# Kernel optimization log

Measured on AMD Instinct MI355X. Metric: run time of the kernel, lower is better.

The kernel has to match this reference:

```python
import jax, jax.numpy as jnp
import numpy as np

H1, H2 = 32, 16  # LSTM units per direction (layer 1, layer 2)
F = 64           # input feature dim


def lstm(x, W, U, b, reverse=False, return_sequences=True):
    """Keras-style LSTM. x: [B,T,F]. W:[F,4H], U:[H,4H], b:[4H].
    Gate order i,f,g,o; sigmoid recurrent activation, tanh activation.
    Dropout is inference-mode (identity). If reverse, process time backwards
    (go_backwards=True)."""
    if reverse:
        x = x[:, ::-1]
    B = x.shape[0]
    H = U.shape[0]
    xW = jnp.einsum('btf,fg->btg', x, W) + b  # [B,T,4H] precomputed input gates

    def step(carry, xw_t):
        h, c = carry
        z = xw_t + h @ U                       # [B,4H]
        i, f, g, o = jnp.split(z, 4, axis=-1)
        i = jax.nn.sigmoid(i)
        f = jax.nn.sigmoid(f)
        g = jnp.tanh(g)
        o = jax.nn.sigmoid(o)
        c = f * c + i * g
        h = o * jnp.tanh(c)
        return (h, c), h

    h0 = jnp.zeros((B, H), x.dtype)
    (h_last, _), hs = jax.lax.scan(step, (h0, h0), jnp.swapaxes(xW, 0, 1))
    if return_sequences:
        hs = jnp.swapaxes(hs, 0, 1)  # [B,T,H]
        if reverse:
            hs = hs[:, ::-1]  # Bidirectional re-reverses backward outputs
        return hs
    return h_last


def setup_inputs() -> dict:
    key = jax.random.key(0)
    ks = jax.random.split(key, 17)
    s = 0.05
    d = {
        'inputs': jax.random.normal(ks[0], (4096, 128, F), jnp.float32),
        # layer 1 (bidirectional, 32 units each dir)
        'W1f': jax.random.normal(ks[1], (F, 4 * H1)) * s,
        'U1f': jax.random.normal(ks[2], (H1, 4 * H1)) * s,
        'b1f': jnp.zeros((4 * H1,)),
        'W1b': jax.random.normal(ks[3], (F, 4 * H1)) * s,
        'U1b': jax.random.normal(ks[4], (H1, 4 * H1)) * s,
        'b1b': jnp.zeros((4 * H1,)),
        # layer 2 (bidirectional, 16 units each dir, input 2*H1=64)
        'W2f': jax.random.normal(ks[5], (2 * H1, 4 * H2)) * s,
        'U2f': jax.random.normal(ks[6], (H2, 4 * H2)) * s,
        'b2f': jnp.zeros((4 * H2,)),
        'W2b': jax.random.normal(ks[7], (2 * H1, 4 * H2)) * s,
        'U2b': jax.random.normal(ks[8], (H2, 4 * H2)) * s,
        'b2b': jnp.zeros((4 * H2,)),
        # dense head
        'W3': jax.random.normal(ks[9], (2 * H2, 8)) * s,
        'b3': jnp.zeros((8,)),
        'W4': jax.random.normal(ks[10], (8, 2)) * s,
        'b4': jnp.zeros((2,)),
    }
    return d


def reference(inputs, W1f, U1f, b1f, W1b, U1b, b1b,
              W2f, U2f, b2f, W2b, U2b, b2b, W3, b3, W4, b4):
    # bi_one: concat(forward seq, time-aligned backward seq) -> [B,T,64]
    h1f = lstm(inputs, W1f, U1f, b1f, reverse=False, return_sequences=True)
    h1b = lstm(inputs, W1b, U1b, b1b, reverse=True, return_sequences=True)
    x = jnp.concatenate([h1f, h1b], axis=-1)
    # bi_two: last hidden state of each direction -> [B,32]
    h2f = lstm(x, W2f, U2f, b2f, reverse=False, return_sequences=False)
    h2b = lstm(x, W2b, U2b, b2b, reverse=True, return_sequences=False)
    x = jnp.concatenate([h2f, h2b], axis=-1)
    x = x @ W3 + b3
    x = x * jax.nn.sigmoid(x)  # swish
    x = x @ W4 + b4
    return jax.nn.sigmoid(x)
```

## Files before the change

### kernel.cpp

```cpp
#include <hip/hip_runtime.h>
#include <hip/hip_bf16.h>

#define T 128
#define F 64
#define H1 32
#define G1 128
#define H2 16
#define G2 64

typedef __attribute__((ext_vector_type(8))) short bf16x8;
typedef __attribute__((ext_vector_type(4))) float f32x4;

__device__ __forceinline__ float sigmoidf_(float x) {
    return 1.0f / (1.0f + __expf(-x));
}
__device__ __forceinline__ float tanhf_(float x) {
    return 1.0f - 2.0f / (__expf(2.0f * x) + 1.0f);
}
__device__ __forceinline__ unsigned short f2bf(float f) {
    union { float f; unsigned u; } c; c.f = f;
    unsigned r = c.u + 0x7FFF + ((c.u >> 16) & 1);
    return (unsigned short)(r >> 16);
}
__device__ __forceinline__ void lds_barrier() {
    asm volatile("s_waitcnt lgkmcnt(0)" ::: "memory");
    __builtin_amdgcn_s_barrier();
}

__global__ __launch_bounds__(256) void xcvt(
    const float* __restrict__ x,
    unsigned short* __restrict__ xbf)
{
    __shared__ unsigned short tile[1024];
    const int g  = blockIdx.x;
    const int t0 = blockIdx.y * 8;
    const int m  = threadIdx.x >> 4;
    const int c4 = threadIdx.x & 15;
    const int ks   = c4 >> 3;
    const int quad = (c4 & 7) >> 1;
    const int j0   = (c4 & 1) * 4;
    const int slot = ks * 512 + (m + 16 * quad) * 8 + j0;

    for (int tt = 0; tt < 8; ++tt) {
        const int t = t0 + tt;
        const float4 v = *(const float4*)(x + ((size_t)(g * 16 + m) * T + t) * 64 + c4 * 4);
        ushort4 u;
        u.x = f2bf(v.x); u.y = f2bf(v.y); u.z = f2bf(v.z); u.w = f2bf(v.w);
        *(ushort4*)(tile + slot) = u;
        __syncthreads();
        *(uint2*)(xbf + (size_t)(g * T + t) * 1024 + threadIdx.x * 4) =
            *(const uint2*)(tile + threadIdx.x * 4);
        __syncthreads();
    }
}

__global__ __launch_bounds__(256, 2) void lstm1_fused(
    const unsigned short* __restrict__ xbf,
    const float* __restrict__ W1f, const float* __restrict__ b1f, const float* __restrict__ U1f,
    const float* __restrict__ W1b, const float* __restrict__ b1b, const float* __restrict__ U1b,
    unsigned short* __restrict__ h1)
{
    __shared__ unsigned short hb[2][16 * 40];
    const int tid  = threadIdx.x;
    const int lane = tid & 63;
    const int wv   = __builtin_amdgcn_readfirstlane(tid >> 6);
    const int gh   = wv & 1;
    const int sh   = wv >> 1;
    const int n15  = lane & 15, quad = lane >> 4;
    const int d    = blockIdx.x & 1, g = blockIdx.x >> 1;

    const float* W  = d ? W1b : W1f;
    const float* U  = d ? U1b : U1f;
    const float* bs = d ? b1b : b1f;

    bf16x8 Wf[4][2], Uf[4];
    f32x4 biasC[4];
    #pragma unroll
    for (int i = 0; i < 4; ++i) {
        const int col = (2 * i + gh) * 16 + n15;
        biasC[i] = (f32x4)(bs[col]);
        #pragma unroll
        for (int ks = 0; ks < 2; ++ks) {
            bf16x8 f;
            #pragma unroll
            for (int j = 0; j < 8; ++j)
                f[j] = (short)f2bf(W[(ks * 32 + quad * 8 + j) * G1 + col]);
            Wf[i][ks] = f;
        }
        bf16x8 u;
        #pragma unroll
        for (int j = 0; j < 8; ++j)
            u[j] = (short)f2bf(U[(quad * 8 + j) * G1 + col]);
        Uf[i] = u;
    }

    #pragma unroll
    for (int i = 0; i < 5; ++i) ((unsigned short*)hb)[tid + i * 256] = 0;

    float c0 = 0.0f, c1 = 0.0f;
    const unsigned short* xb = xbf + (size_t)g * T * 1024 + lane * 8;
    unsigned short* h1b0 = h1 + (size_t)g * T * 1024
        + d * 512 + ((quad * 4 + 2 * sh) + 16 * (gh * 2 + (n15 >> 3))) * 8 + (n15 & 7);
    unsigned short* h1b1 = h1b0 + 8;

    bf16x8 xA0, xA1, xB0, xB1;
    {
        const unsigned short* p0 = xb + (size_t)(d ? (T - 1) : 0) * 1024;
        xA0 = *(const bf16x8*)(p0); xA1 = *(const bf16x8*)(p0 + 512);
        const unsigned short* p1 = xb + (size_t)(d ? (T - 2) : 1) * 1024;
        xB0 = *(const bf16x8*)(p1); xB1 = *(const bf16x8*)(p1 + 512);
    }
    lds_barrier();

    auto step = [&](int s, bf16x8& x0, bf16x8& x1) {
        const int t = d ? (T - 1 - s) : s;
        f32x4 a0 = __builtin_amdgcn_mfma_f32_16x16x32_bf16(x0, Wf[0][0], biasC[0], 0, 0, 0);
        f32x4 a1 = __builtin_amdgcn_mfma_f32_16x16x32_bf16(x0, Wf[1][0], biasC[1], 0, 0, 0);
        f32x4 a2 = __builtin_amdgcn_mfma_f32_16x16x32_bf16(x0, Wf[2][0], biasC[2], 0, 0, 0);
        f32x4 a3 = __builtin_amdgcn_mfma_f32_16x16x32_bf16(x0, Wf[3][0], biasC[3], 0, 0, 0);
        a0 = __builtin_amdgcn_mfma_f32_16x16x32_bf16(x1, Wf[0][1], a0, 0, 0, 0);
        a1 = __builtin_amdgcn_mfma_f32_16x16x32_bf16(x1, Wf[1][1], a1, 0, 0, 0);
        a2 = __builtin_amdgcn_mfma_f32_16x16x32_bf16(x1, Wf[2][1], a2, 0, 0, 0);
        a3 = __builtin_amdgcn_mfma_f32_16x16x32_bf16(x1, Wf[3][1], a3, 0, 0, 0);

        if (s + 2 < T) {
            const unsigned short* pn = xb + (size_t)(d ? (T - 3 - s) : (s + 2)) * 1024;
            x0 = *(const bf16x8*)(pn); x1 = *(const bf16x8*)(pn + 512);
        }

        const bf16x8 af = *(const bf16x8*)(hb[s & 1] + n15 * 40 + quad * 8);
        a0 = __builtin_amdgcn_mfma_f32_16x16x32_bf16(af, Uf[0], a0, 0, 0, 0);
        a1 = __builtin_amdgcn_mfma_f32_16x16x32_bf16(af, Uf[1], a1, 0, 0, 0);
        a2 = __builtin_amdgcn_mfma_f32_16x16x32_bf16(af, Uf[2], a2, 0, 0, 0);
        a3 = __builtin_amdgcn_mfma_f32_16x16x32_bf16(af, Uf[3], a3, 0, 0, 0);

        {
            const float ig = sigmoidf_(sh ? a0[2] : a0[0]);
            const float fg = sigmoidf_(sh ? a1[2] : a1[0]);
            const float gg = tanhf_(sh ? a2[2] : a2[0]);
            const float og = sigmoidf_(sh ? a3[2] : a3[0]);
            c0 = fg * c0 + ig * gg;
            const float h = og * tanhf_(c0);
            const unsigned short us = f2bf(h);
            hb[(s + 1) & 1][(quad * 4 + 2 * sh) * 40 + gh * 16 + n15] = us;
            h1b0[(size_t)t * 1024] = us;
        }
        {
            const float ig = sigmoidf_(sh ? a0[3] : a0[1]);
            const float fg = sigmoidf_(sh ? a1[3] : a1[1]);
            const float gg = tanhf_(sh ? a2[3] : a2[1]);
            const float og = sigmoidf_(sh ? a3[3] : a3[1]);
            c1 = fg * c1 + ig * gg;
            const float h = og * tanhf_(c1);
            const unsigned short us = f2bf(h);
            hb[(s + 1) & 1][(quad * 4 + 2 * sh + 1) * 40 + gh * 16 + n15] = us;
            h1b1[(size_t)t * 1024] = us;
        }
        lds_barrier();
    };

    #pragma unroll 1
    for (int s = 0; s < T; s += 2) {
        step(s, xA0, xA1);
        step(s + 1, xB0, xB1);
    }
}

__global__ __launch_bounds__(512, 2) void lstm2_head(
    const unsigned short* __restrict__ h1,
    const float* __restrict__ W2f, const float* __restrict__ b2f, const float* __restrict__ U2f,
    const float* __restrict__ W2b, const float* __restrict__ b2b, const float* __restrict__ U2b,
    const float* __restrict__ W3, const float* __restrict__ b3,
    const float* __restrict__ W4, const float* __restrict__ b4,
    float* __restrict__ out)
{
    __shared__ unsigned short hb2[2][2][400];
    __shared__ float hfin[2][16][16];
    __shared__ float ybuf[16][9];
    const int tid  = threadIdx.x;
    const int lane = tid & 63;
    const int wv   = __builtin_amdgcn_readfirstlane(tid >> 6);
    const int d    = wv & 1;
    const int sh   = wv >> 1;
    const int n15  = lane & 15, quad = lane >> 4;
    const int g    = blockIdx.x;

    const float* W  = d ? W2b : W2f;
    const float* U  = d ? U2b : U2f;
    const float* bs = d ? b2b : b2f;

    bf16x8 Wf[4][2], Uf[4];
    f32x4 biasC[4];
    #pragma unroll
    for (int i = 0; i < 4; ++i) {
        const int col = i * 16 + n15;
        biasC[i] = (f32x4)(bs[col]);
        #pragma unroll
        for (int ks = 0; ks < 2; ++ks) {
            bf16x8 f;
            #pragma unroll
            for (int j = 0; j < 8; ++j)
                f[j] = (short)f2bf(W[(ks * 32 + quad * 8 + j) * G2 + col]);
            Wf[i][ks] = f;
        }
        bf16x8 u;
        #pragma unroll
        for (int j = 0; j < 8; ++j) {
            const int k = quad * 8 + j;
            u[j] = (k < H2) ? (short)f2bf(U[k * G2 + col]) : (short)0;
        }
        Uf[i] = u;
    }

    #pragma unroll
    for (int i = 0; i < 4; ++i) {
        const int idx = tid + i * 512;
        if (idx < 1600) ((unsigned short*)hb2)[idx] = 0;
    }

    float c = 0.0f, hlast = 0.0f;
    const unsigned short* hl = h1 + (size_t)g * T * 1024 + lane * 8;

    bf16x8 hA0, hA1, hB0, hB1;
    {
        const unsigned short* p0 = hl + (size_t)(d ? (T - 1) : 0) * 1024;
        hA0 = *(const bf16x8*)(p0); hA1 = *(const bf16x8*)(p0 + 512);
        const unsigned short* p1 = hl + (size_t)(d ? (T - 2) : 1) * 1024;
        hB0 = *(const bf16x8*)(p1); hB1 = *(const bf16x8*)(p1 + 512);
    }
    lds_barrier();

    auto step = [&](int s, bf16x8& x0, bf16x8& x1) {
        f32x4 a0 = __builtin_amdgcn_mfma_f32_16x16x32_bf16(x0, Wf[0][0], biasC[0], 0, 0, 0);
        f32x4 a1 = __builtin_amdgcn_mfma_f32_16x16x32_bf16(x0, Wf[1][0], biasC[1], 0, 0, 0);
        f32x4 a2 = __builtin_amdgcn_mfma_f32_16x16x32_bf16(x0, Wf[2][0], biasC[2], 0, 0, 0);
        f32x4 a3 = __builtin_amdgcn_mfma_f32_16x16x32_bf16(x0, Wf[3][0], biasC[3], 0, 0, 0);
        a0 = __builtin_amdgcn_mfma_f32_16x16x32_bf16(x1, Wf[0][1], a0, 0, 0, 0);
        a1 = __builtin_amdgcn_mfma_f32_16x16x32_bf16(x1, Wf[1][1], a1, 0, 0, 0);
        a2 = __builtin_amdgcn_mfma_f32_16x16x32_bf16(x1, Wf[2][1], a2, 0, 0, 0);
        a3 = __builtin_amdgcn_mfma_f32_16x16x32_bf16(x1, Wf[3][1], a3, 0, 0, 0);

        if (s + 2 < T) {
            const unsigned short* pn = hl + (size_t)(d ? (T - 3 - s) : (s + 2)) * 1024;
            x0 = *(const bf16x8*)(pn); x1 = *(const bf16x8*)(pn + 512);
        }

        const bf16x8 af = *(const bf16x8*)(hb2[d][s & 1] + n15 * 24 + quad * 8);
        a0 = __builtin_amdgcn_mfma_f32_16x16x32_bf16(af, Uf[0], a0, 0, 0, 0);
        a1 = __builtin_amdgcn_mfma_f32_16x16x32_bf16(af, Uf[1], a1, 0, 0, 0);
        a2 = __builtin_amdgcn_mfma_f32_16x16x32_bf16(af, Uf[2], a2, 0, 0, 0);
        a3 = __builtin_amdgcn_mfma_f32_16x16x32_bf16(af, Uf[3], a3, 0, 0, 0);

        const float z0 = (sh & 1) ? ((sh & 2) ? a0[3] : a0[1]) : ((sh & 2) ? a0[2] : a0[0]);
        const float z1 = (sh & 1) ? ((sh & 2) ? a1[3] : a1[1]) : ((sh & 2) ? a1[2] : a1[0]);
        const float z2 = (sh & 1) ? ((sh & 2) ? a2[3] : a2[1]) : ((sh & 2) ? a2[2] : a2[0]);
        const float z3 = (sh & 1) ? ((sh & 2) ? a3[3] : a3[1]) : ((sh & 2) ? a3[2] : a3[0]);
        const float ig = sigmoidf_(z0);
        const float fg = sigmoidf_(z1);
        const float gg = tanhf_(z2);
        const float og = sigmoidf_(z3);
        c = fg * c + ig * gg;
        hlast = og * tanhf_(c);
        hb2[d][(s + 1) & 1][(quad * 4 + sh) * 24 + n15] = f2bf(hlast);
        lds_barrier();
    };

    #pragma unroll 1
    for (int s = 0; s < T; s += 2) {
        step(s, hA0, hA1);
        step(s + 1, hB0, hB1);
    }

    hfin[d][quad * 4 + sh][n15] = hlast;
    __syncthreads();

    if (tid < 128) {
        const int s = tid >> 3, u = tid & 7;
        float a = b3[u];
        #pragma unroll
        for (int k = 0; k < H2; ++k) a += hfin[0][s][k] * W3[k * 8 + u];
        #pragma unroll
        for (int k = 0; k < H2; ++k) a += hfin[1][s][k] * W3[(H2 + k) * 8 + u];
        ybuf[s][u] = a * sigmoidf_(a);
    }
    __syncthreads();
    if (tid < 32) {
        const int s = tid >> 1, o = tid & 1;
        float a = b4[o];
        #pragma unroll
        for (int k = 0; k < 8; ++k) a += ybuf[s][k] * W4[k * 2 + o];
        out[(size_t)(g * 16 + s) * 2 + o] = sigmoidf_(a);
    }
}

extern "C" void kernel_launch(void* const* d_in, const int* in_sizes, int n_in,
                              void* d_out, int out_size, void* d_ws, size_t ws_size,
                              hipStream_t stream) {
    const float* x   = (const float*)d_in[0];
    const float* W1f = (const float*)d_in[1];
    const float* U1f = (const float*)d_in[2];
    const float* b1f = (const float*)d_in[3];
    const float* W1b = (const float*)d_in[4];
    const float* U1b = (const float*)d_in[5];
    const float* b1b = (const float*)d_in[6];
    const float* W2f = (const float*)d_in[7];
    const float* U2f = (const float*)d_in[8];
    const float* b2f = (const float*)d_in[9];
    const float* W2b = (const float*)d_in[10];
    const float* U2b = (const float*)d_in[11];
    const float* b2b = (const float*)d_in[12];
    const float* W3  = (const float*)d_in[13];
    const float* b3  = (const float*)d_in[14];
    const float* W4  = (const float*)d_in[15];
    const float* b4  = (const float*)d_in[16];
    float* out = (float*)d_out;

    const int B  = in_sizes[0] / (T * F);
    const int NG = B / 16;

    const size_t perG = (size_t)T * 1024 * sizeof(unsigned short);
    int chG = (int)(ws_size / (2 * perG));
    if (chG > NG) chG = NG;
    if (chG < 1) chG = 1;
    unsigned short* xbf = (unsigned short*)d_ws;
    unsigned short* h1  = xbf + (size_t)chG * T * 1024;

    for (int g0 = 0; g0 < NG; g0 += chG) {
        const int cg = (NG - g0 < chG) ? (NG - g0) : chG;
        dim3 gcv(cg, T / 8);
        xcvt<<<gcv, 256, 0, stream>>>(x + (size_t)g0 * 16 * T * F, xbf);
        lstm1_fused<<<cg * 2, 256, 0, stream>>>(
            xbf, W1f, b1f, U1f, W1b, b1b, U1b, h1);
        lstm2_head<<<cg, 512, 0, stream>>>(
            h1, W2f, b2f, U2f, W2b, b2b, U2b, W3, b3, W4, b4,
            out + (size_t)g0 * 16 * 2);
    }
}
```

Measured before the change: 428.1 us.

## Software-pipeline input projection MFMAs one step ahead of recurrent chain

Both LSTM kernels now compute the input projection x·W for step s+2 while step s's recurrent h·U MFMAs and gate math run. This takes those MFMAs off the serial per-step critical path, and the input prefetch distance grows to four steps. Sigmoid and tanh now use the hardware reciprocal instead of a division, and gate element selection uses branches on sh instead of nested selects. The cost is more accumulator registers per lane and slightly lower precision in the activations.

Result: faster. 383.4 us (-10.4%).

```diff
diff --git a/kernel.cpp b/kernel.cpp
--- a/kernel.cpp
+++ b/kernel.cpp
@@ -12,10 +12,10 @@
 typedef __attribute__((ext_vector_type(4))) float f32x4;
 
 __device__ __forceinline__ float sigmoidf_(float x) {
-    return 1.0f / (1.0f + __expf(-x));
+    return __builtin_amdgcn_rcpf(1.0f + __expf(-x));
 }
 __device__ __forceinline__ float tanhf_(float x) {
-    return 1.0f - 2.0f / (__expf(2.0f * x) + 1.0f);
+    return 1.0f - 2.0f * __builtin_amdgcn_rcpf(__expf(2.0f * x) + 1.0f);
 }
 __device__ __forceinline__ unsigned short f2bf(float f) {
     union { float f; unsigned u; } c; c.f = f;
@@ -103,42 +103,65 @@
         + d * 512 + ((quad * 4 + 2 * sh) + 16 * (gh * 2 + (n15 >> 3))) * 8 + (n15 & 7);
     unsigned short* h1b1 = h1b0 + 8;
 
+    f32x4 xaA[4], xaB[4];
     bf16x8 xA0, xA1, xB0, xB1;
     {
         const unsigned short* p0 = xb + (size_t)(d ? (T - 1) : 0) * 1024;
-        xA0 = *(const bf16x8*)(p0); xA1 = *(const bf16x8*)(p0 + 512);
+        bf16x8 t0 = *(const bf16x8*)(p0), t1 = *(const bf16x8*)(p0 + 512);
+        #pragma unroll
+        for (int i = 0; i < 4; ++i) {
+            xaA[i] = __builtin_amdgcn_mfma_f32_16x16x32_bf16(t0, Wf[i][0], biasC[i], 0, 0, 0);
+            xaA[i] = __builtin_amdgcn_mfma_f32_16x16x32_bf16(t1, Wf[i][1], xaA[i], 0, 0, 0);
+        }
         const unsigned short* p1 = xb + (size_t)(d ? (T - 2) : 1) * 1024;
-        xB0 = *(const bf16x8*)(p1); xB1 = *(const bf16x8*)(p1 + 512);
+        t0 = *(const bf16x8*)(p1); t1 = *(const bf16x8*)(p1 + 512);
+        #pragma unroll
+        for (int i = 0; i < 4; ++i) {
+            xaB[i] = __builtin_amdgcn_mfma_f32_16x16x32_bf16(t0, Wf[i][0], biasC[i], 0, 0, 0);
+            xaB[i] = __builtin_amdgcn_mfma_f32_16x16x32_bf16(t1, Wf[i][1], xaB[i], 0, 0, 0);
+        }
+        const unsigned short* p2 = xb + (size_t)(d ? (T - 3) : 2) * 1024;
+        xA0 = *(const bf16x8*)(p2); xA1 = *(const bf16x8*)(p2 + 512);
+        const unsigned short* p3 = xb + (size_t)(d ? (T - 4) : 3) * 1024;
+        xB0 = *(const bf16x8*)(p3); xB1 = *(const bf16x8*)(p3 + 512);
     }
     lds_barrier();
 
-    auto step = [&](int s, bf16x8& x0, bf16x8& x1) {
+    auto step = [&](int s, f32x4* xa, bf16x8& x0, bf16x8& x1) {
+        const bf16x8 af = *(const bf16x8*)(hb[s & 1] + n15 * 40 + quad * 8);
+        f32x4 a0 = __builtin_amdgcn_mfma_f32_16x16x32_bf16(af, Uf[0], xa[0], 0, 0, 0);
+        f32x4 a1 = __builtin_amdgcn_mfma_f32_16x16x32_bf16(af, Uf[1], xa[1], 0, 0, 0);
+        f32x4 a2 = __builtin_amdgcn_mfma_f32_16x16x32_bf16(af, Uf[2], xa[2], 0, 0, 0);
+        f32x4 a3 = __builtin_amdgcn_mfma_f32_16x16x32_bf16(af, Uf[3], xa[3], 0, 0, 0);
+
+        xa[0] = __builtin_amdgcn_mfma_f32_16x16x32_bf16(x0, Wf[0][0], biasC[0], 0, 0, 0);
+        xa[1] = __builtin_amdgcn_mfma_f32_16x16x32_bf16(x0, Wf[1][0], biasC[1], 0, 0, 0);
+        xa[2] = __builtin_amdgcn_mfma_f32_16x16x32_bf16(x0, Wf[2][0], biasC[2], 0, 0, 0);
+        xa[3] = __builtin_amdgcn_mfma_f32_16x16x32_bf16(x0, Wf[3][0], biasC[3], 0, 0, 0);
+        xa[0] = __builtin_amdgcn_mfma_f32_16x16x32_bf16(x1, Wf[0][1], xa[0], 0, 0, 0);
+        xa[1] = __builtin_amdgcn_mfma_f32_16x16x32_bf16(x1, Wf[1][1], xa[1], 0, 0, 0);
+        xa[2] = __builtin_amdgcn_mfma_f32_16x16x32_bf16(x1, Wf[2][1], xa[2], 0, 0, 0);
+        xa[3] = __builtin_amdgcn_mfma_f32_16x16x32_bf16(x1, Wf[3][1], xa[3], 0, 0, 0);
+
+        if (s + 4 < T) {
+            const unsigned short* pn = xb + (size_t)(d ? (T - 5 - s) : (s + 4)) * 1024;
+            x0 = *(const bf16x8*)(pn); x1 = *(const bf16x8*)(pn + 512);
+        }
+
         const int t = d ? (T - 1 - s) : s;
-        f32x4 a0 = __builtin_amdgcn_mfma_f32_16x16x32_bf16(x0, Wf[0][0], biasC[0], 0, 0, 0);
-        f32x4 a1 = __builtin_amdgcn_mfma_f32_16x16x32_bf16(x0, Wf[1][0], biasC[1], 0, 0, 0);
-        f32x4 a2 = __builtin_amdgcn_mfma_f32_16x16x32_bf16(x0, Wf[2][0], biasC[2], 0, 0, 0);
-        f32x4 a3 = __builtin_amdgcn_mfma_f32_16x16x32_bf16(x0, Wf[3][0], biasC[3], 0, 0, 0);
-        a0 = __builtin_amdgcn_mfma_f32_16x16x32_bf16(x1, Wf[0][1], a0, 0, 0, 0);
-        a1 = __builtin_amdgcn_mfma_f32_16x16x32_bf16(x1, Wf[1][1], a1, 0, 0, 0);
-        a2 = __builtin_amdgcn_mfma_f32_16x16x32_bf16(x1, Wf[2][1], a2, 0, 0, 0);
-        a3 = __builtin_amdgcn_mfma_f32_16x16x32_bf16(x1, Wf[3][1], a3, 0, 0, 0);
-
-        if (s + 2 < T) {
-            const unsigned short* pn = xb + (size_t)(d ? (T - 3 - s) : (s + 2)) * 1024;
-            x0 = *(const bf16x8*)(pn); x1 = *(const bf16x8*)(pn + 512);
-        }
-
-        const bf16x8 af = *(const bf16x8*)(hb[s & 1] + n15 * 40 + quad * 8);
-        a0 = __builtin_amdgcn_mfma_f32_16x16x32_bf16(af, Uf[0], a0, 0, 0, 0);
-        a1 = __builtin_amdgcn_mfma_f32_16x16x32_bf16(af, Uf[1], a1, 0, 0, 0);
-        a2 = __builtin_amdgcn_mfma_f32_16x16x32_bf16(af, Uf[2], a2, 0, 0, 0);
-        a3 = __builtin_amdgcn_mfma_f32_16x16x32_bf16(af, Uf[3], a3, 0, 0, 0);
-
+        float zi0, zi1, zf0, zf1, zg0, zg1, zo0, zo1;
+        if (sh == 0) {
+            zi0 = a0[0]; zi1 = a0[1]; zf0 = a1[0]; zf1 = a1[1];
+            zg0 = a2[0]; zg1 = a2[1]; zo0 = a3[0]; zo1 = a3[1];
+        } else {
+            zi0 = a0[2]; zi1 = a0[3]; zf0 = a1[2]; zf1 = a1[3];
+            zg0 = a2[2]; zg1 = a2[3]; zo0 = a3[2]; zo1 = a3[3];
+        }
         {
-            const float ig = sigmoidf_(sh ? a0[2] : a0[0]);
-            const float fg = sigmoidf_(sh ? a1[2] : a1[0]);
-            const float gg = tanhf_(sh ? a2[2] : a2[0]);
-            const float og = sigmoidf_(sh ? a3[2] : a3[0]);
+            const float ig = sigmoidf_(zi0);
+            const float fg = sigmoidf_(zf0);
+            const float gg = tanhf_(zg0);
+            const float og = sigmoidf_(zo0);
             c0 = fg * c0 + ig * gg;
             const float h = og * tanhf_(c0);
             const unsigned short us = f2bf(h);
@@ -146,10 +169,10 @@
             h1b0[(size_t)t * 1024] = us;
         }
         {
-            const float ig = sigmoidf_(sh ? a0[3] : a0[1]);
-            const float fg = sigmoidf_(sh ? a1[3] : a1[1]);
-            const float gg = tanhf_(sh ? a2[3] : a2[1]);
-            const float og = sigmoidf_(sh ? a3[3] : a3[1]);
+            const float ig = sigmoidf_(zi1);
+            const float fg = sigmoidf_(zf1);
+            const float gg = tanhf_(zg1);
+            const float og = sigmoidf_(zo1);
             c1 = fg * c1 + ig * gg;
             const float h = og * tanhf_(c1);
             const unsigned short us = f2bf(h);
@@ -161,8 +184,8 @@
 
     #pragma unroll 1
     for (int s = 0; s < T; s += 2) {
-        step(s, xA0, xA1);
-        step(s + 1, xB0, xB1);
+        step(s, xaA, xA0, xA1);
+        step(s + 1, xaB, xB0, xB1);
     }
 }
 
@@ -221,40 +244,56 @@
     float c = 0.0f, hlast = 0.0f;
     const unsigned short* hl = h1 + (size_t)g * T * 1024 + lane * 8;
 
+    f32x4 xaA[4], xaB[4];
     bf16x8 hA0, hA1, hB0, hB1;
     {
         const unsigned short* p0 = hl + (size_t)(d ? (T - 1) : 0) * 1024;
-        hA0 = *(const bf16x8*)(p0); hA1 = *(const bf16x8*)(p0 + 512);
+        bf16x8 t0 = *(const bf16x8*)(p0), t1 = *(const bf16x8*)(p0 + 512);
+        #pragma unroll
+        for (int i = 0; i < 4; ++i) {
+            xaA[i] = __builtin_amdgcn_mfma_f32_16x16x32_bf16(t0, Wf[i][0], biasC[i], 0, 0, 0);
+            xaA[i] = __builtin_amdgcn_mfma_f32_16x16x32_bf16(t1, Wf[i][1], xaA[i], 0, 0, 0);
+        }
         const unsigned short* p1 = hl + (size_t)(d ? (T - 2) : 1) * 1024;
-        hB0 = *(const bf16x8*)(p1); hB1 = *(const bf16x8*)(p1 + 512);
+        t0 = *(const bf16x8*)(p1); t1 = *(const bf16x8*)(p1 + 512);
+        #pragma unroll
+        for (int i = 0; i < 4; ++i) {
+            xaB[i] = __builtin_amdgcn_mfma_f32_16x16x32_bf16(t0, Wf[i][0], biasC[i], 0, 0, 0);
+            xaB[i] = __builtin_amdgcn_mfma_f32_16x16x32_bf16(t1, Wf[i][1], xaB[i], 0, 0, 0);
+        }
+        const unsigned short* p2 = hl + (size_t)(d ? (T - 3) : 2) * 1024;
+        hA0 = *(const bf16x8*)(p2); hA1 = *(const bf16x8*)(p2 + 512);
+        const unsigned short* p3 = hl + (size_t)(d ? (T - 4) : 3) * 1024;
+        hB0 = *(const bf16x8*)(p3); hB1 = *(const bf16x8*)(p3 + 512);
     }
     lds_barrier();
 
-    auto step = [&](int s, bf16x8& x0, bf16x8& x1) {
-        f32x4 a0 = __builtin_amdgcn_mfma_f32_16x16x32_bf16(x0, Wf[0][0], biasC[0], 0, 0, 0);
-        f32x4 a1 = __builtin_amdgcn_mfma_f32_16x16x32_bf16(x0, Wf[1][0], biasC[1], 0, 0, 0);
-        f32x4 a2 = __builtin_amdgcn_mfma_f32_16x16x32_bf16(x0, Wf[2][0], biasC[2], 0, 0, 0);
-        f32x4 a3 = __builtin_amdgcn_mfma_f32_16x16x32_bf16(x0, Wf[3][0], biasC[3], 0, 0, 0);
-        a0 = __builtin_amdgcn_mfma_f32_16x16x32_bf16(x1, Wf[0][1], a0, 0, 0, 0);
-        a1 = __builtin_amdgcn_mfma_f32_16x16x32_bf16(x1, Wf[1][1], a1, 0, 0, 0);
-        a2 = __builtin_amdgcn_mfma_f32_16x16x32_bf16(x1, Wf[2][1], a2, 0, 0, 0);
-        a3 = __builtin_amdgcn_mfma_f32_16x16x32_bf16(x1, Wf[3][1], a3, 0, 0, 0);
-
-        if (s + 2 < T) {
-            const unsigned short* pn = hl + (size_t)(d ? (T - 3 - s) : (s + 2)) * 1024;
+    auto step = [&](int s, f32x4* xa, bf16x8& x0, bf16x8& x1) {
+        const bf16x8 af = *(const bf16x8*)(hb2[d][s & 1] + n15 * 24 + quad * 8);
+        f32x4 a0 = __builtin_amdgcn_mfma_f32_16x16x32_bf16(af, Uf[0], xa[0], 0, 0, 0);
+        f32x4 a1 = __builtin_amdgcn_mfma_f32_16x16x32_bf16(af, Uf[1], xa[1], 0, 0, 0);
+        f32x4 a2 = __builtin_amdgcn_mfma_f32_16x16x32_bf16(af, Uf[2], xa[2], 0, 0, 0);
+        f32x4 a3 = __builtin_amdgcn_mfma_f32_16x16x32_bf16(af, Uf[3], xa[3], 0, 0, 0);
+
+        xa[0] = __builtin_amdgcn_mfma_f32_16x16x32_bf16(x0, Wf[0][0], biasC[0], 0, 0, 0);
+        xa[1] = __builtin_amdgcn_mfma_f32_16x16x32_bf16(x0, Wf[1][0], biasC[1], 0, 0, 0);
+        xa[2] = __builtin_amdgcn_mfma_f32_16x16x32_bf16(x0, Wf[2][0], biasC[2], 0, 0, 0);
+        xa[3] = __builtin_amdgcn_mfma_f32_16x16x32_bf16(x0, Wf[3][0], biasC[3], 0, 0, 0);
+        xa[0] = __builtin_amdgcn_mfma_f32_16x16x32_bf16(x1, Wf[0][1], xa[0], 0, 0, 0);
+        xa[1] = __builtin_amdgcn_mfma_f32_16x16x32_bf16(x1, Wf[1][1], xa[1], 0, 0, 0);
+        xa[2] = __builtin_amdgcn_mfma_f32_16x16x32_bf16(x1, Wf[2][1], xa[2], 0, 0, 0);
+        xa[3] = __builtin_amdgcn_mfma_f32_16x16x32_bf16(x1, Wf[3][1], xa[3], 0, 0, 0);
+
+        if (s + 4 < T) {
+            const unsigned short* pn = hl + (size_t)(d ? (T - 5 - s) : (s + 4)) * 1024;
             x0 = *(const bf16x8*)(pn); x1 = *(const bf16x8*)(pn + 512);
         }
 
-        const bf16x8 af = *(const bf16x8*)(hb2[d][s & 1] + n15 * 24 + quad * 8);
-        a0 = __builtin_amdgcn_mfma_f32_16x16x32_bf16(af, Uf[0], a0, 0, 0, 0);
-        a1 = __builtin_amdgcn_mfma_f32_16x16x32_bf16(af, Uf[1], a1, 0, 0, 0);
-        a2 = __builtin_amdgcn_mfma_f32_16x16x32_bf16(af, Uf[2], a2, 0, 0, 0);
-        a3 = __builtin_amdgcn_mfma_f32_16x16x32_bf16(af, Uf[3], a3, 0, 0, 0);
-
-        const float z0 = (sh & 1) ? ((sh & 2) ? a0[3] : a0[1]) : ((sh & 2) ? a0[2] : a0[0]);
-        const float z1 = (sh & 1) ? ((sh & 2) ? a1[3] : a1[1]) : ((sh & 2) ? a1[2] : a1[0]);
-        const float z2 = (sh & 1) ? ((sh & 2) ? a2[3] : a2[1]) : ((sh & 2) ? a2[2] : a2[0]);
-        const float z3 = (sh & 1) ? ((sh & 2) ? a3[3] : a3[1]) : ((sh & 2) ? a3[2] : a3[0]);
+        float z0, z1, z2, z3;
+        if (sh == 0)      { z0 = a0[0]; z1 = a1[0]; z2 = a2[0]; z3 = a3[0]; }
+        else if (sh == 1) { z0 = a0[1]; z1 = a1[1]; z2 = a2[1]; z3 = a3[1]; }
+        else if (sh == 2) { z0 = a0[2]; z1 = a1[2]; z2 = a2[2]; z3 = a3[2]; }
+        else              { z0 = a0[3]; z1 = a1[3]; z2 = a2[3]; z3 = a3[3]; }
         const float ig = sigmoidf_(z0);
         const float fg = sigmoidf_(z1);
         const float gg = tanhf_(z2);
@@ -267,8 +306,8 @@
 
     #pragma unroll 1
     for (int s = 0; s < T; s += 2) {
-        step(s, hA0, hA1);
-        step(s + 1, hB0, hB1);
+        step(s, xaA, hA0, hA1);
+        step(s + 1, xaB, hB0, hB1);
     }
 
     hfin[d][quad * 4 + sh][n15] = hlast;
```

## Interleave two batch groups per LSTM block and split head into its own kernel

Applied to the files above, without the earlier changes.

Each recurrent block now processes two independent 16-sample groups, so the MFMA and activation latency of one group can overlap the other within a single serial timestep. The input projection for the next step is computed after the recurrent MFMA, which takes it off the critical path. Layer 2 is split per direction into 256-thread blocks, and the dense head runs as a separate kernel that reads final states from the workspace. Other changes: the conversion kernel drops its LDS staging, and the activations use reciprocal intrinsics. The trade-offs are fewer blocks overall, occupancy of one block per CU, higher register pressure, and an extra kernel launch.

Measured after the change: 479.5 us. 12.0% more time.

```diff
diff --git a/kernel.cpp b/kernel.cpp
--- a/kernel.cpp
+++ b/kernel.cpp
@@ -11,11 +11,13 @@
 typedef __attribute__((ext_vector_type(8))) short bf16x8;
 typedef __attribute__((ext_vector_type(4))) float f32x4;
 
+#define MFMA __builtin_amdgcn_mfma_f32_16x16x32_bf16
+
 __device__ __forceinline__ float sigmoidf_(float x) {
-    return 1.0f / (1.0f + __expf(-x));
+    return __builtin_amdgcn_rcpf(1.0f + __expf(-x));
 }
 __device__ __forceinline__ float tanhf_(float x) {
-    return 1.0f - 2.0f / (__expf(2.0f * x) + 1.0f);
+    return 1.0f - 2.0f * __builtin_amdgcn_rcpf(__expf(2.0f * x) + 1.0f);
 }
 __device__ __forceinline__ unsigned short f2bf(float f) {
     union { float f; unsigned u; } c; c.f = f;
@@ -31,43 +33,37 @@
     const float* __restrict__ x,
     unsigned short* __restrict__ xbf)
 {
-    __shared__ unsigned short tile[1024];
-    const int g  = blockIdx.x;
-    const int t0 = blockIdx.y * 8;
-    const int m  = threadIdx.x >> 4;
-    const int c4 = threadIdx.x & 15;
-    const int ks   = c4 >> 3;
-    const int quad = (c4 & 7) >> 1;
-    const int j0   = (c4 & 1) * 4;
-    const int slot = ks * 512 + (m + 16 * quad) * 8 + j0;
-
-    for (int tt = 0; tt < 8; ++tt) {
-        const int t = t0 + tt;
-        const float4 v = *(const float4*)(x + ((size_t)(g * 16 + m) * T + t) * 64 + c4 * 4);
-        ushort4 u;
-        u.x = f2bf(v.x); u.y = f2bf(v.y); u.z = f2bf(v.z); u.w = f2bf(v.w);
-        *(ushort4*)(tile + slot) = u;
-        __syncthreads();
-        *(uint2*)(xbf + (size_t)(g * T + t) * 1024 + threadIdx.x * 4) =
-            *(const uint2*)(tile + threadIdx.x * 4);
-        __syncthreads();
-    }
-}
-
-__global__ __launch_bounds__(256, 2) void lstm1_fused(
+    const int g = blockIdx.x;
+    const int t = blockIdx.y * 2 + (threadIdx.x >> 7);
+    const int r = threadIdx.x & 127;
+    const int m = r & 15, ks = (r >> 4) & 1, q = r >> 5;
+    const float* src = x + ((size_t)(g * 16 + m) * T + t) * 64 + ks * 32 + q * 8;
+    const float4 v0 = *(const float4*)src;
+    const float4 v1 = *(const float4*)(src + 4);
+    bf16x8 u;
+    u[0] = (short)f2bf(v0.x); u[1] = (short)f2bf(v0.y);
+    u[2] = (short)f2bf(v0.z); u[3] = (short)f2bf(v0.w);
+    u[4] = (short)f2bf(v1.x); u[5] = (short)f2bf(v1.y);
+    u[6] = (short)f2bf(v1.z); u[7] = (short)f2bf(v1.w);
+    *(bf16x8*)(xbf + (size_t)(g * T + t) * 1024 + ks * 512 + (m + 16 * q) * 8) = u;
+}
+
+__global__ __launch_bounds__(256, 1) void lstm1_fused(
     const unsigned short* __restrict__ xbf,
     const float* __restrict__ W1f, const float* __restrict__ b1f, const float* __restrict__ U1f,
     const float* __restrict__ W1b, const float* __restrict__ b1b, const float* __restrict__ U1b,
-    unsigned short* __restrict__ h1)
+    unsigned short* __restrict__ h1, const int ng)
 {
-    __shared__ unsigned short hb[2][16 * 40];
+    __shared__ unsigned short hb[2][2][640];
     const int tid  = threadIdx.x;
     const int lane = tid & 63;
     const int wv   = __builtin_amdgcn_readfirstlane(tid >> 6);
     const int gh   = wv & 1;
     const int sh   = wv >> 1;
     const int n15  = lane & 15, quad = lane >> 4;
-    const int d    = blockIdx.x & 1, g = blockIdx.x >> 1;
+    const int d    = blockIdx.x & 1, gp = blockIdx.x >> 1;
+    const int g0   = gp * 2;
+    const int g1   = (g0 + 1 < ng) ? (g0 + 1) : g0;
 
     const float* W  = d ? W1b : W1f;
     const float* U  = d ? U1b : U1f;
@@ -95,95 +91,108 @@
     }
 
     #pragma unroll
-    for (int i = 0; i < 5; ++i) ((unsigned short*)hb)[tid + i * 256] = 0;
-
-    float c0 = 0.0f, c1 = 0.0f;
-    const unsigned short* xb = xbf + (size_t)g * T * 1024 + lane * 8;
-    unsigned short* h1b0 = h1 + (size_t)g * T * 1024
-        + d * 512 + ((quad * 4 + 2 * sh) + 16 * (gh * 2 + (n15 >> 3))) * 8 + (n15 & 7);
-    unsigned short* h1b1 = h1b0 + 8;
-
-    bf16x8 xA0, xA1, xB0, xB1;
-    {
-        const unsigned short* p0 = xb + (size_t)(d ? (T - 1) : 0) * 1024;
-        xA0 = *(const bf16x8*)(p0); xA1 = *(const bf16x8*)(p0 + 512);
-        const unsigned short* p1 = xb + (size_t)(d ? (T - 2) : 1) * 1024;
-        xB0 = *(const bf16x8*)(p1); xB1 = *(const bf16x8*)(p1 + 512);
+    for (int i = 0; i < 10; ++i) ((unsigned short*)hb)[tid + i * 256] = 0;
+
+    float c0[2] = {0.f, 0.f}, c1[2] = {0.f, 0.f};
+    const unsigned short* xb[2];
+    unsigned short* hw[2];
+    xb[0] = xbf + (size_t)g0 * T * 1024 + lane * 8;
+    xb[1] = xbf + (size_t)g1 * T * 1024 + lane * 8;
+    const int hoff = d * 512
+        + ((quad * 4 + 2 * sh) + 16 * (gh * 2 + (n15 >> 3))) * 8 + (n15 & 7);
+    hw[0] = h1 + (size_t)g0 * T * 1024 + hoff;
+    hw[1] = h1 + (size_t)g1 * T * 1024 + hoff;
+
+    f32x4 xa[2][4];
+    bf16x8 xP0[2], xP1[2];
+    #pragma unroll
+    for (int S = 0; S < 2; ++S) {
+        const unsigned short* p0 = xb[S] + (size_t)(d ? (T - 1) : 0) * 1024;
+        const bf16x8 t0 = *(const bf16x8*)p0, t1 = *(const bf16x8*)(p0 + 512);
+        #pragma unroll
+        for (int i = 0; i < 4; ++i) {
+            xa[S][i] = MFMA(t0, Wf[i][0], biasC[i], 0, 0, 0);
+            xa[S][i] = MFMA(t1, Wf[i][1], xa[S][i], 0, 0, 0);
+        }
+        const unsigned short* p1 = xb[S] + (size_t)(d ? (T - 2) : 1) * 1024;
+        xP0[S] = *(const bf16x8*)p1;
+        xP1[S] = *(const bf16x8*)(p1 + 512);
     }
     lds_barrier();
 
-    auto step = [&](int s, bf16x8& x0, bf16x8& x1) {
+    #pragma unroll 1
+    for (int s = 0; s < T; ++s) {
         const int t = d ? (T - 1 - s) : s;
-        f32x4 a0 = __builtin_amdgcn_mfma_f32_16x16x32_bf16(x0, Wf[0][0], biasC[0], 0, 0, 0);
-        f32x4 a1 = __builtin_amdgcn_mfma_f32_16x16x32_bf16(x0, Wf[1][0], biasC[1], 0, 0, 0);
-        f32x4 a2 = __builtin_amdgcn_mfma_f32_16x16x32_bf16(x0, Wf[2][0], biasC[2], 0, 0, 0);
-        f32x4 a3 = __builtin_amdgcn_mfma_f32_16x16x32_bf16(x0, Wf[3][0], biasC[3], 0, 0, 0);
-        a0 = __builtin_amdgcn_mfma_f32_16x16x32_bf16(x1, Wf[0][1], a0, 0, 0, 0);
-        a1 = __builtin_amdgcn_mfma_f32_16x16x32_bf16(x1, Wf[1][1], a1, 0, 0, 0);
-        a2 = __builtin_amdgcn_mfma_f32_16x16x32_bf16(x1, Wf[2][1], a2, 0, 0, 0);
-        a3 = __builtin_amdgcn_mfma_f32_16x16x32_bf16(x1, Wf[3][1], a3, 0, 0, 0);
-
-        if (s + 2 < T) {
-            const unsigned short* pn = xb + (size_t)(d ? (T - 3 - s) : (s + 2)) * 1024;
-            x0 = *(const bf16x8*)(pn); x1 = *(const bf16x8*)(pn + 512);
-        }
-
-        const bf16x8 af = *(const bf16x8*)(hb[s & 1] + n15 * 40 + quad * 8);
-        a0 = __builtin_amdgcn_mfma_f32_16x16x32_bf16(af, Uf[0], a0, 0, 0, 0);
-        a1 = __builtin_amdgcn_mfma_f32_16x16x32_bf16(af, Uf[1], a1, 0, 0, 0);
-        a2 = __builtin_amdgcn_mfma_f32_16x16x32_bf16(af, Uf[2], a2, 0, 0, 0);
-        a3 = __builtin_amdgcn_mfma_f32_16x16x32_bf16(af, Uf[3], a3, 0, 0, 0);
-
-        {
-            const float ig = sigmoidf_(sh ? a0[2] : a0[0]);
-            const float fg = sigmoidf_(sh ? a1[2] : a1[0]);
-            const float gg = tanhf_(sh ? a2[2] : a2[0]);
-            const float og = sigmoidf_(sh ? a3[2] : a3[0]);
-            c0 = fg * c0 + ig * gg;
-            const float h = og * tanhf_(c0);
-            const unsigned short us = f2bf(h);
-            hb[(s + 1) & 1][(quad * 4 + 2 * sh) * 40 + gh * 16 + n15] = us;
-            h1b0[(size_t)t * 1024] = us;
-        }
-        {
-            const float ig = sigmoidf_(sh ? a0[3] : a0[1]);
-            const float fg = sigmoidf_(sh ? a1[3] : a1[1]);
-            const float gg = tanhf_(sh ? a2[3] : a2[1]);
-            const float og = sigmoidf_(sh ? a3[3] : a3[1]);
-            c1 = fg * c1 + ig * gg;
-            const float h = og * tanhf_(c1);
-            const unsigned short us = f2bf(h);
-            hb[(s + 1) & 1][(quad * 4 + 2 * sh + 1) * 40 + gh * 16 + n15] = us;
-            h1b1[(size_t)t * 1024] = us;
+        f32x4 a[2][4];
+        #pragma unroll
+        for (int S = 0; S < 2; ++S) {
+            const bf16x8 af = *(const bf16x8*)(hb[S][s & 1] + n15 * 40 + quad * 8);
+            #pragma unroll
+            for (int i = 0; i < 4; ++i)
+                a[S][i] = MFMA(af, Uf[i], xa[S][i], 0, 0, 0);
+        }
+        #pragma unroll
+        for (int S = 0; S < 2; ++S) {
+            #pragma unroll
+            for (int i = 0; i < 4; ++i)
+                xa[S][i] = MFMA(xP0[S], Wf[i][0], biasC[i], 0, 0, 0);
+            #pragma unroll
+            for (int i = 0; i < 4; ++i)
+                xa[S][i] = MFMA(xP1[S], Wf[i][1], xa[S][i], 0, 0, 0);
+            if (s + 2 < T) {
+                const unsigned short* pn =
+                    xb[S] + (size_t)(d ? (T - 3 - s) : (s + 2)) * 1024;
+                xP0[S] = *(const bf16x8*)pn;
+                xP1[S] = *(const bf16x8*)(pn + 512);
+            }
+        }
+        #pragma unroll
+        for (int S = 0; S < 2; ++S) {
+            float zi0, zi1, zf0, zf1, zg0, zg1, zo0, zo1;
+            if (sh == 0) {
+                zi0 = a[S][0][0]; zi1 = a[S][0][1]; zf0 = a[S][1][0]; zf1 = a[S][1][1];
+                zg0 = a[S][2][0]; zg1 = a[S][2][1]; zo0 = a[S][3][0]; zo1 = a[S][3][1];
+            } else {
+                zi0 = a[S][0][2]; zi1 = a[S][0][3]; zf0 = a[S][1][2]; zf1 = a[S][1][3];
+                zg0 = a[S][2][2]; zg1 = a[S][2][3]; zo0 = a[S][3][2]; zo1 = a[S][3][3];
+            }
+            {
+                const float ig = sigmoidf_(zi0), fg = sigmoidf_(zf0);
+                const float gg = tanhf_(zg0),   og = sigmoidf_(zo0);
+                c0[S] = fg * c0[S] + ig * gg;
+                const float h = og * tanhf_(c0[S]);
+                const unsigned short us = f2bf(h);
+                hb[S][(s + 1) & 1][(quad * 4 + 2 * sh) * 40 + gh * 16 + n15] = us;
+                hw[S][(size_t)t * 1024] = us;
+            }
+            {
+                const float ig = sigmoidf_(zi1), fg = sigmoidf_(zf1);
+                const float gg = tanhf_(zg1),   og = sigmoidf_(zo1);
+                c1[S] = fg * c1[S] + ig * gg;
+                const float h = og * tanhf_(c1[S]);
+                const unsigned short us = f2bf(h);
+                hb[S][(s + 1) & 1][(quad * 4 + 2 * sh + 1) * 40 + gh * 16 + n15] = us;
+                hw[S][(size_t)t * 1024 + 8] = us;
+            }
         }
         lds_barrier();
-    };
-
-    #pragma unroll 1
-    for (int s = 0; s < T; s += 2) {
-        step(s, xA0, xA1);
-        step(s + 1, xB0, xB1);
-    }
-}
-
-__global__ __launch_bounds__(512, 2) void lstm2_head(
+    }
+}
+
+__global__ __launch_bounds__(256, 1) void lstm2_rec(
     const unsigned short* __restrict__ h1,
     const float* __restrict__ W2f, const float* __restrict__ b2f, const float* __restrict__ U2f,
     const float* __restrict__ W2b, const float* __restrict__ b2b, const float* __restrict__ U2b,
-    const float* __restrict__ W3, const float* __restrict__ b3,
-    const float* __restrict__ W4, const float* __restrict__ b4,
-    float* __restrict__ out)
+    float* __restrict__ hfin, const int ng)
 {
     __shared__ unsigned short hb2[2][2][400];
-    __shared__ float hfin[2][16][16];
-    __shared__ float ybuf[16][9];
     const int tid  = threadIdx.x;
     const int lane = tid & 63;
-    const int wv   = __builtin_amdgcn_readfirstlane(tid >> 6);
-    const int d    = wv & 1;
-    const int sh   = wv >> 1;
+    const int sh   = __builtin_amdgcn_readfirstlane(tid >> 6);
     const int n15  = lane & 15, quad = lane >> 4;
-    const int g    = blockIdx.x;
+    const int d    = blockIdx.x & 1, gp = blockIdx.x >> 1;
+    const int g0   = gp * 2;
+    const int g1   = (g0 + 1 < ng) ? (g0 + 1) : g0;
 
     const float* W  = d ? W2b : W2f;
     const float* U  = d ? U2b : U2f;
@@ -213,83 +222,104 @@
     }
 
     #pragma unroll
-    for (int i = 0; i < 4; ++i) {
-        const int idx = tid + i * 512;
+    for (int i = 0; i < 7; ++i) {
+        const int idx = tid + i * 256;
         if (idx < 1600) ((unsigned short*)hb2)[idx] = 0;
     }
 
-    float c = 0.0f, hlast = 0.0f;
-    const unsigned short* hl = h1 + (size_t)g * T * 1024 + lane * 8;
-
-    bf16x8 hA0, hA1, hB0, hB1;
-    {
-        const unsigned short* p0 = hl + (size_t)(d ? (T - 1) : 0) * 1024;
-        hA0 = *(const bf16x8*)(p0); hA1 = *(const bf16x8*)(p0 + 512);
-        const unsigned short* p1 = hl + (size_t)(d ? (T - 2) : 1) * 1024;
-        hB0 = *(const bf16x8*)(p1); hB1 = *(const bf16x8*)(p1 + 512);
+    float c[2] = {0.f, 0.f}, hlast[2] = {0.f, 0.f};
+    const unsigned short* hl[2];
+    hl[0] = h1 + (size_t)g0 * T * 1024 + lane * 8;
+    hl[1] = h1 + (size_t)g1 * T * 1024 + lane * 8;
+
+    f32x4 xa[2][4];
+    bf16x8 xP0[2], xP1[2];
+    #pragma unroll
+    for (int S = 0; S < 2; ++S) {
+        const unsigned short* p0 = hl[S] + (size_t)(d ? (T - 1) : 0) * 1024;
+        const bf16x8 t0 = *(const bf16x8*)p0, t1 = *(const bf16x8*)(p0 + 512);
+        #pragma unroll
+        for (int i = 0; i < 4; ++i) {
+            xa[S][i] = MFMA(t0, Wf[i][0], biasC[i], 0, 0, 0);
+            xa[S][i] = MFMA(t1, Wf[i][1], xa[S][i], 0, 0, 0);
+        }
+        const unsigned short* p1 = hl[S] + (size_t)(d ? (T - 2) : 1) * 1024;
+        xP0[S] = *(const bf16x8*)p1;
+        xP1[S] = *(const bf16x8*)(p1 + 512);
     }
     lds_barrier();
 
-    auto step = [&](int s, bf16x8& x0, bf16x8& x1) {
-        f32x4 a0 = __builtin_amdgcn_mfma_f32_16x16x32_bf16(x0, Wf[0][0], biasC[0], 0, 0, 0);
-        f32x4 a1 = __builtin_amdgcn_mfma_f32_16x16x32_bf16(x0, Wf[1][0], biasC[1], 0, 0, 0);
-        f32x4 a2 = __builtin_amdgcn_mfma_f32_16x16x32_bf16(x0, Wf[2][0], biasC[2], 0, 0, 0);
-        f32x4 a3 = __builtin_amdgcn_mfma_f32_16x16x32_bf16(x0, Wf[3][0], biasC[3], 0, 0, 0);
-        a0 = __builtin_amdgcn_mfma_f32_16x16x32_bf16(x1, Wf[0][1], a0, 0, 0, 0);
-        a1 = __builtin_amdgcn_mfma_f32_16x16x32_bf16(x1, Wf[1][1], a1, 0, 0, 0);
-        a2 = __builtin_amdgcn_mfma_f32_16x16x32_bf16(x1, Wf[2][1], a2, 0, 0, 0);
-        a3 = __builtin_amdgcn_mfma_f32_16x16x32_bf16(x1, Wf[3][1], a3, 0, 0, 0);
-
-        if (s + 2 < T) {
-            const unsigned short* pn = hl + (size_t)(d ? (T - 3 - s) : (s + 2)) * 1024;
-            x0 = *(const bf16x8*)(pn); x1 = *(const bf16x8*)(pn + 512);
-        }
-
-        const bf16x8 af = *(const bf16x8*)(hb2[d][s & 1] + n15 * 24 + quad * 8);
-        a0 = __builtin_amdgcn_mfma_f32_16x16x32_bf16(af, Uf[0], a0, 0, 0, 0);
-        a1 = __builtin_amdgcn_mfma_f32_16x16x32_bf16(af, Uf[1], a1, 0, 0, 0);
-        a2 = __builtin_amdgcn_mfma_f32_16x16x32_bf16(af, Uf[2], a2, 0, 0, 0);
-        a3 = __builtin_amdgcn_mfma_f32_16x16x32_bf16(af, Uf[3], a3, 0, 0, 0);
-
-        const float z0 = (sh & 1) ? ((sh & 2) ? a0[3] : a0[1]) : ((sh & 2) ? a0[2] : a0[0]);
-        const float z1 = (sh & 1) ? ((sh & 2) ? a1[3] : a1[1]) : ((sh & 2) ? a1[2] : a1[0]);
-        const float z2 = (sh & 1) ? ((sh & 2) ? a2[3] : a2[1]) : ((sh & 2) ? a2[2] : a2[0]);
-        const float z3 = (sh & 1) ? ((sh & 2) ? a3[3] : a3[1]) : ((sh & 2) ? a3[2] : a3[0]);
-        const float ig = sigmoidf_(z0);
-        const float fg = sigmoidf_(z1);
-        const float gg = tanhf_(z2);
-        const float og = sigmoidf_(z3);
-        c = fg * c + ig * gg;
-        hlast = og * tanhf_(c);
-        hb2[d][(s + 1) & 1][(quad * 4 + sh) * 24 + n15] = f2bf(hlast);
+    #pragma unroll 1
+    for (int s = 0; s < T; ++s) {
+        f32x4 a[2][4];
+        #pragma unroll
+        for (int S = 0; S < 2; ++S) {
+            const bf16x8 af = *(const bf16x8*)(hb2[S][s & 1] + n15 * 24 + quad * 8);
+            #pragma unroll
+            for (int i = 0; i < 4; ++i)
+                a[S][i] = MFMA(af, Uf[i], xa[S][i], 0, 0, 0);
+        }
+        #pragma unroll
+        for (int S = 0; S < 2; ++S) {
+            #pragma unroll
+            for (int i = 0; i < 4; ++i)
+                xa[S][i] = MFMA(xP0[S], Wf[i][0], biasC[i], 0, 0, 0);
+            #pragma unroll
+            for (int i = 0; i < 4; ++i)
+                xa[S][i] = MFMA(xP1[S], Wf[i][1], xa[S][i], 0, 0, 0);
+            if (s + 2 < T) {
+                const unsigned short* pn =
+                    hl[S] + (size_t)(d ? (T - 3 - s) : (s + 2)) * 1024;
+                xP0[S] = *(const bf16x8*)pn;
+                xP1[S] = *(const bf16x8*)(pn + 512);
+            }
+        }
+        #pragma unroll
+        for (int S = 0; S < 2; ++S) {
+            float z0, z1, z2, z3;
+            if (sh == 0)      { z0 = a[S][0][0]; z1 = a[S][1][0]; z2 = a[S][2][0]; z3 = a[S][3][0]; }
+            else if (sh == 1) { z0 = a[S][0][1]; z1 = a[S][1][1]; z2 = a[S][2][1]; z3 = a[S][3][1]; }
+            else if (sh == 2) { z0 = a[S][0][2]; z1 = a[S][1][2]; z2 = a[S][2][2]; z3 = a[S][3][2]; }
+            else              { z0 = a[S][0][3]; z1 = a[S][1][3]; z2 = a[S][2][3]; z3 = a[S][3][3]; }
+            const float ig = sigmoidf_(z0), fg = sigmoidf_(z1);
+            const float gg = tanhf_(z2),   og = sigmoidf_(z3);
+            c[S] = fg * c[S] + ig * gg;
+            hlast[S] = og * tanhf_(c[S]);
+            hb2[S][(s + 1) & 1][(quad * 4 + sh) * 24 + n15] = f2bf(hlast[S]);
+        }
         lds_barrier();
-    };
-
-    #pragma unroll 1
-    for (int s = 0; s < T; s += 2) {
-        step(s, hA0, hA1);
-        step(s + 1, hB0, hB1);
-    }
-
-    hfin[d][quad * 4 + sh][n15] = hlast;
-    __syncthreads();
-
-    if (tid < 128) {
-        const int s = tid >> 3, u = tid & 7;
+    }
+
+    hfin[((size_t)(g0 * 16 + quad * 4 + sh)) * 32 + d * 16 + n15] = hlast[0];
+    hfin[((size_t)(g1 * 16 + quad * 4 + sh)) * 32 + d * 16 + n15] = hlast[1];
+}
+
+__global__ __launch_bounds__(256) void head(
+    const float* __restrict__ hfin,
+    const float* __restrict__ W3, const float* __restrict__ b3,
+    const float* __restrict__ W4, const float* __restrict__ b4,
+    float* __restrict__ out, const int ns)
+{
+    const int i = blockIdx.x * 256 + threadIdx.x;
+    if (i >= ns) return;
+    float h[32];
+    #pragma unroll
+    for (int k = 0; k < 8; ++k)
+        *(float4*)(h + k * 4) = *(const float4*)(hfin + (size_t)i * 32 + k * 4);
+    float y[8];
+    #pragma unroll
+    for (int u = 0; u < 8; ++u) {
         float a = b3[u];
         #pragma unroll
-        for (int k = 0; k < H2; ++k) a += hfin[0][s][k] * W3[k * 8 + u];
-        #pragma unroll
-        for (int k = 0; k < H2; ++k) a += hfin[1][s][k] * W3[(H2 + k) * 8 + u];
-        ybuf[s][u] = a * sigmoidf_(a);
-    }
-    __syncthreads();
-    if (tid < 32) {
-        const int s = tid >> 1, o = tid & 1;
+        for (int k = 0; k < 32; ++k) a += h[k] * W3[k * 8 + u];
+        y[u] = a * sigmoidf_(a);
+    }
+    #pragma unroll
+    for (int o = 0; o < 2; ++o) {
         float a = b4[o];
         #pragma unroll
-        for (int k = 0; k < 8; ++k) a += ybuf[s][k] * W4[k * 2 + o];
-        out[(size_t)(g * 16 + s) * 2 + o] = sigmoidf_(a);
+        for (int u = 0; u < 8; ++u) a += y[u] * W4[u * 2 + o];
+        out[(size_t)i * 2 + o] = sigmoidf_(a);
     }
 }
 
@@ -327,12 +357,14 @@
 
     for (int g0 = 0; g0 < NG; g0 += chG) {
         const int cg = (NG - g0 < chG) ? (NG - g0) : chG;
-        dim3 gcv(cg, T / 8);
+        dim3 gcv(cg, T / 2);
         xcvt<<<gcv, 256, 0, stream>>>(x + (size_t)g0 * 16 * T * F, xbf);
-        lstm1_fused<<<cg * 2, 256, 0, stream>>>(
-            xbf, W1f, b1f, U1f, W1b, b1b, U1b, h1);
-        lstm2_head<<<cg, 512, 0, stream>>>(
-            h1, W2f, b2f, U2f, W2b, b2b, U2b, W3, b3, W4, b4,
-            out + (size_t)g0 * 16 * 2);
-    }
-}
+        const int np = (cg + 1) / 2;
+        lstm1_fused<<<np * 2, 256, 0, stream>>>(
+            xbf, W1f, b1f, U1f, W1b, b1b, U1b, h1, cg);
+        lstm2_rec<<<np * 2, 256, 0, stream>>>(
+            h1, W2f, b2f, U2f, W2b, b2b, U2b, (float*)xbf, cg);
+        head<<<(cg * 16 + 255) / 256, 256, 0, stream>>>(
+            (float*)xbf, W3, b3, W4, b4, out + (size_t)g0 * 16 * 2, cg * 16);
+    }
+}
```
